# Kernel optimization log

Measured on AMD Instinct MI355X. Metric: run time of the kernel, lower is better.

Reference implementation:

```python
import jax, jax.numpy as jnp
import numpy as np

GAMMA = 0.99   # discount_factor
LAM = 0.95     # smoothing_factor

def setup_inputs() -> dict:
    key = jax.random.key(0)
    k1, k2, k3, k4 = jax.random.split(key, 4)
    B, T = 4096, 2048
    return {
        "rewards": jax.random.normal(k1, (B, T), dtype=jnp.float32),
        "values": jax.random.normal(k2, (B, T), dtype=jnp.float32),
        "next_value": jax.random.normal(k3, (B,), dtype=jnp.float32),
        "done_flags": jax.random.randint(k4, (B, T), 0, 2, dtype=jnp.int32),
    }

def reference(rewards, values, next_value, done_flags):
    d = done_flags.astype(rewards.dtype)
    # next_non_terminal[t] = 1 - done[t+1] for t < T-1, and 1 - done[T-1] at t = T-1
    nnt = 1.0 - jnp.concatenate([d[..., 1:], d[..., -1:]], axis=-1)
    # next value at step t: values[t+1] for t < T-1, bootstrap next_value at t = T-1
    nv = jnp.concatenate([values[..., 1:], next_value[..., None]], axis=-1)
    delta = rewards + GAMMA * nv * nnt - values  # [B, T]

    def step(gae, x):
        dl, nn = x
        gae = dl + GAMMA * LAM * nn * gae
        return gae, gae

    # scan backward over time (leading axis for lax.scan)
    deltaT = jnp.moveaxis(delta, -1, 0)  # [T, B]
    nntT = jnp.moveaxis(nnt, -1, 0)      # [T, B]
    init = jnp.zeros(rewards.shape[:-1], rewards.dtype)
    _, advT = jax.lax.scan(step, init, (deltaT, nntT), reverse=True)
    advantages = jnp.moveaxis(advT, 0, -1)  # [B, T]
    returns = advantages + values
    return advantages, returns
```

## Files before the change

### kernel.cpp

```cpp
#include <hip/hip_runtime.h>

#define GAMMA 0.99f
#define LAM   0.95f

typedef float v4f __attribute__((ext_vector_type(4)));
typedef int   v4i __attribute__((ext_vector_type(4)));

constexpr int CH   = 8;
constexpr int SEG  = 64 * CH;
constexpr int NSEG = 4;
constexpr int WPB  = 4;

struct Raw {
    v4f ra, rb, va, vb;
    v4i da, db;
};

__device__ __forceinline__ Raw load_seg(const float* __restrict__ r,
                                        const float* __restrict__ v,
                                        const int*   __restrict__ d,
                                        long base) {
    Raw x;
    x.ra = reinterpret_cast<const v4f*>(r + base)[0];
    x.rb = reinterpret_cast<const v4f*>(r + base)[1];
    x.va = reinterpret_cast<const v4f*>(v + base)[0];
    x.vb = reinterpret_cast<const v4f*>(v + base)[1];
    x.da = reinterpret_cast<const v4i*>(d + base)[0];
    x.db = reinterpret_cast<const v4i*>(d + base)[1];
    return x;
}

__device__ __forceinline__ void compute_seg(
    const Raw x, const int lane, const bool last_seg, const float nvrow,
    float& g, float& bv, int& bd,
    float* __restrict__ adv_out, float* __restrict__ ret_out, const long base)
{
    float r[CH] = {x.ra.x, x.ra.y, x.ra.z, x.ra.w, x.rb.x, x.rb.y, x.rb.z, x.rb.w};
    float v[CH] = {x.va.x, x.va.y, x.va.z, x.va.w, x.vb.x, x.vb.y, x.vb.z, x.vb.w};
    int   d[CH] = {x.da.x, x.da.y, x.da.z, x.da.w, x.db.x, x.db.y, x.db.z, x.db.w};

    int   dnext = __shfl_down(d[0], 1);
    float vnext = __shfl_down(v[0], 1);
    if (lane == 63) {
        dnext = last_seg ? d[CH - 1] : bd;
        vnext = last_seg ? nvrow     : bv;
    }
    const float bv_new = __shfl(v[0], 0);
    const int   bd_new = __shfl(d[0], 0);

    float delta[CH], c[CH];
#pragma unroll
    for (int j = 0; j < CH; ++j) {
        const int   dn  = (j < CH - 1) ? d[j + 1] : dnext;
        const float nv  = (j < CH - 1) ? v[j + 1] : vnext;
        const float nnt = dn ? 0.0f : 1.0f;
        delta[j] = r[j] + GAMMA * nv * nnt - v[j];
        c[j]     = dn ? 0.0f : (GAMMA * LAM);
    }

    float a = 0.0f, m = 1.0f;
#pragma unroll
    for (int j = CH - 1; j >= 0; --j) { a = delta[j] + c[j] * a; m = c[j] * m; }

    float sa = a, sm = m;
#pragma unroll
    for (int s = 1; s < 64; s <<= 1) {
        const float oa = __shfl_down(sa, s);
        const float om = __shfl_down(sm, s);
        if (lane + s < 64) { sa += sm * oa; sm *= om; }
    }
    float gin = __shfl_down(sa, 1);
    float em  = __shfl_down(sm, 1);
    if (lane == 63) { gin = 0.0f; em = 1.0f; }
    gin = gin + em * g;

    float adv[CH];
#pragma unroll
    for (int j = CH - 1; j >= 0; --j) { gin = delta[j] + c[j] * gin; adv[j] = gin; }

    v4f* a4 = reinterpret_cast<v4f*>(adv_out + base);
    v4f* t4 = reinterpret_cast<v4f*>(ret_out + base);
    v4f o0; o0.x = adv[0]; o0.y = adv[1]; o0.z = adv[2]; o0.w = adv[3];
    v4f o1; o1.x = adv[4]; o1.y = adv[5]; o1.z = adv[6]; o1.w = adv[7];
    v4f s0; s0.x = adv[0]+v[0]; s0.y = adv[1]+v[1]; s0.z = adv[2]+v[2]; s0.w = adv[3]+v[3];
    v4f s1; s1.x = adv[4]+v[4]; s1.y = adv[5]+v[5]; s1.z = adv[6]+v[6]; s1.w = adv[7]+v[7];
    a4[0] = o0; a4[1] = o1;
    t4[0] = s0; t4[1] = s1;

    g  = __shfl(gin, 0);
    bv = bv_new;
    bd = bd_new;
}

__global__ __launch_bounds__(256, 4) void gae_wave_seg_kernel(
    const float* __restrict__ rewards,
    const float* __restrict__ values,
    const float* __restrict__ next_value,
    const int*   __restrict__ done,
    float* __restrict__ adv_out,
    float* __restrict__ ret_out,
    int B, int T)
{
    const int tid  = threadIdx.x;
    const int lane = tid & 63;
    const int wave = tid >> 6;
    const int row  = blockIdx.x * WPB + wave;
    if (row >= B) return;

    const long rowbase = (long)row * T;
    const long laneoff = rowbase + lane * CH;

    Raw b3 = load_seg(rewards, values, done, laneoff + 3 * SEG);
    Raw b2 = load_seg(rewards, values, done, laneoff + 2 * SEG);
    const float nvrow = next_value[row];

    float g = 0.0f, bv = 0.0f;
    int   bd = 0;

    Raw b1 = load_seg(rewards, values, done, laneoff + 1 * SEG);
    compute_seg(b3, lane, true,  nvrow, g, bv, bd, adv_out, ret_out, laneoff + 3 * SEG);
    Raw b0 = load_seg(rewards, values, done, laneoff + 0 * SEG);
    compute_seg(b2, lane, false, nvrow, g, bv, bd, adv_out, ret_out, laneoff + 2 * SEG);
    compute_seg(b1, lane, false, nvrow, g, bv, bd, adv_out, ret_out, laneoff + 1 * SEG);
    compute_seg(b0, lane, false, nvrow, g, bv, bd, adv_out, ret_out, laneoff + 0 * SEG);
}

__global__ void gae_naive_kernel(
    const float* __restrict__ rewards,
    const float* __restrict__ values,
    const float* __restrict__ next_value,
    const int*   __restrict__ done,
    float* __restrict__ adv_out,
    float* __restrict__ ret_out,
    int B, int T)
{
    int row = blockIdx.x * blockDim.x + threadIdx.x;
    if (row >= B) return;
    long base = (long)row * T;
    float g = 0.0f;
    for (int t = T - 1; t >= 0; --t) {
        int dcol = (t + 1 < T) ? (t + 1) : (T - 1);
        float nnt = 1.0f - (float)done[base + dcol];
        float nv  = (t + 1 < T) ? values[base + t + 1] : next_value[row];
        float dl  = rewards[base + t] + GAMMA * nv * nnt - values[base + t];
        g = dl + (GAMMA * LAM) * nnt * g;
        adv_out[base + t] = g;
        ret_out[base + t] = g + values[base + t];
    }
}

extern "C" void kernel_launch(void* const* d_in, const int* in_sizes, int n_in,
                              void* d_out, int out_size, void* d_ws, size_t ws_size,
                              hipStream_t stream) {
    const float* rewards    = (const float*)d_in[0];
    const float* values     = (const float*)d_in[1];
    const float* next_value = (const float*)d_in[2];
    const int*   done       = (const int*)d_in[3];

    const int B = in_sizes[2];
    const int T = in_sizes[0] / B;

    float* adv = (float*)d_out;
    float* ret = adv + (long)B * T;

    if (T == NSEG * SEG) {
        const int grid = (B + WPB - 1) / WPB;
        gae_wave_seg_kernel<<<grid, 256, 0, stream>>>(
            rewards, values, next_value, done, adv, ret, B, T);
    } else {
        gae_naive_kernel<<<(B + 255) / 256, 256, 0, stream>>>(
            rewards, values, next_value, done, adv, ret, B, T);
    }
}
```

Before: 153.2 us.

## Process two rows per wavefront with interleaved segment scans for ILP

```diff
diff --git a/kernel.cpp b/kernel.cpp
--- a/kernel.cpp
+++ b/kernel.cpp
@@ -9,11 +9,17 @@
 constexpr int CH   = 8;
 constexpr int SEG  = 64 * CH;
 constexpr int NSEG = 4;
-constexpr int WPB  = 4;
+constexpr int RPW  = 2;
 
 struct Raw {
     v4f ra, rb, va, vb;
     v4i da, db;
+};
+
+struct RowState {
+    float g;
+    float bv;
+    int   bd;
 };
 
 __device__ __forceinline__ Raw load_seg(const float* __restrict__ r,
@@ -32,7 +38,7 @@
 
 __device__ __forceinline__ void compute_seg(
     const Raw x, const int lane, const bool last_seg, const float nvrow,
-    float& g, float& bv, int& bd,
+    RowState& st,
     float* __restrict__ adv_out, float* __restrict__ ret_out, const long base)
 {
     float r[CH] = {x.ra.x, x.ra.y, x.ra.z, x.ra.w, x.rb.x, x.rb.y, x.rb.z, x.rb.w};
@@ -42,8 +48,8 @@
     int   dnext = __shfl_down(d[0], 1);
     float vnext = __shfl_down(v[0], 1);
     if (lane == 63) {
-        dnext = last_seg ? d[CH - 1] : bd;
-        vnext = last_seg ? nvrow     : bv;
+        dnext = last_seg ? d[CH - 1] : st.bd;
+        vnext = last_seg ? nvrow     : st.bv;
     }
     const float bv_new = __shfl(v[0], 0);
     const int   bd_new = __shfl(d[0], 0);
@@ -72,7 +78,7 @@
     float gin = __shfl_down(sa, 1);
     float em  = __shfl_down(sm, 1);
     if (lane == 63) { gin = 0.0f; em = 1.0f; }
-    gin = gin + em * g;
+    gin = gin + em * st.g;
 
     float adv[CH];
 #pragma unroll
@@ -87,12 +93,12 @@
     a4[0] = o0; a4[1] = o1;
     t4[0] = s0; t4[1] = s1;
 
-    g  = __shfl(gin, 0);
-    bv = bv_new;
-    bd = bd_new;
+    st.g  = __shfl(gin, 0);
+    st.bv = bv_new;
+    st.bd = bd_new;
 }
 
-__global__ __launch_bounds__(256, 4) void gae_wave_seg_kernel(
+__global__ __launch_bounds__(256, 2) void gae_wave2_kernel(
     const float* __restrict__ rewards,
     const float* __restrict__ values,
     const float* __restrict__ next_value,
@@ -104,25 +110,39 @@
     const int tid  = threadIdx.x;
     const int lane = tid & 63;
     const int wave = tid >> 6;
-    const int row  = blockIdx.x * WPB + wave;
-    if (row >= B) return;
+    const int gw   = blockIdx.x * 4 + wave;
+    const int row0 = gw * RPW;
+    const int row1 = row0 + 1;
+    if (row0 >= B) return;
+    const bool has1 = (row1 < B);
 
-    const long rowbase = (long)row * T;
-    const long laneoff = rowbase + lane * CH;
+    const long off0 = (long)row0 * T + lane * CH;
+    const long off1 = (long)row1 * T + lane * CH;
 
-    Raw b3 = load_seg(rewards, values, done, laneoff + 3 * SEG);
-    Raw b2 = load_seg(rewards, values, done, laneoff + 2 * SEG);
-    const float nvrow = next_value[row];
+    Raw a3 = load_seg(rewards, values, done, off0 + 3 * SEG);
+    Raw b3 = has1 ? load_seg(rewards, values, done, off1 + 3 * SEG) : Raw{};
+    Raw a2 = load_seg(rewards, values, done, off0 + 2 * SEG);
+    Raw b2 = has1 ? load_seg(rewards, values, done, off1 + 2 * SEG) : Raw{};
+    const float nv0 = next_value[row0];
+    const float nv1 = has1 ? next_value[row1] : 0.0f;
 
-    float g = 0.0f, bv = 0.0f;
-    int   bd = 0;
+    RowState s0 = {0.0f, 0.0f, 0};
+    RowState s1 = {0.0f, 0.0f, 0};
 
-    Raw b1 = load_seg(rewards, values, done, laneoff + 1 * SEG);
-    compute_seg(b3, lane, true,  nvrow, g, bv, bd, adv_out, ret_out, laneoff + 3 * SEG);
-    Raw b0 = load_seg(rewards, values, done, laneoff + 0 * SEG);
-    compute_seg(b2, lane, false, nvrow, g, bv, bd, adv_out, ret_out, laneoff + 2 * SEG);
-    compute_seg(b1, lane, false, nvrow, g, bv, bd, adv_out, ret_out, laneoff + 1 * SEG);
-    compute_seg(b0, lane, false, nvrow, g, bv, bd, adv_out, ret_out, laneoff + 0 * SEG);
+    compute_seg(a3, lane, true, nv0, s0, adv_out, ret_out, off0 + 3 * SEG);
+    Raw a1 = load_seg(rewards, values, done, off0 + 1 * SEG);
+    if (has1) compute_seg(b3, lane, true, nv1, s1, adv_out, ret_out, off1 + 3 * SEG);
+    Raw b1 = has1 ? load_seg(rewards, values, done, off1 + 1 * SEG) : Raw{};
+
+    compute_seg(a2, lane, false, nv0, s0, adv_out, ret_out, off0 + 2 * SEG);
+    Raw a0 = load_seg(rewards, values, done, off0 + 0 * SEG);
+    if (has1) compute_seg(b2, lane, false, nv1, s1, adv_out, ret_out, off1 + 2 * SEG);
+    Raw b0 = has1 ? load_seg(rewards, values, done, off1 + 0 * SEG) : Raw{};
+
+    compute_seg(a1, lane, false, nv0, s0, adv_out, ret_out, off0 + 1 * SEG);
+    if (has1) compute_seg(b1, lane, false, nv1, s1, adv_out, ret_out, off1 + 1 * SEG);
+    compute_seg(a0, lane, false, nv0, s0, adv_out, ret_out, off0 + 0 * SEG);
+    if (has1) compute_seg(b0, lane, false, nv1, s1, adv_out, ret_out, off1 + 0 * SEG);
 }
 
 __global__ void gae_naive_kernel(
@@ -164,8 +184,9 @@
     float* ret = adv + (long)B * T;
 
     if (T == NSEG * SEG) {
-        const int grid = (B + WPB - 1) / WPB;
-        gae_wave_seg_kernel<<<grid, 256, 0, stream>>>(
+        const int nwaves = (B + RPW - 1) / RPW;
+        const int grid   = (nwaves + 3) / 4;
+        gae_wave2_kernel<<<grid, 256, 0, stream>>>(
             rewards, values, next_value, done, adv, ret, B, T);
     } else {
         gae_naive_kernel<<<(B + 255) / 256, 256, 0, stream>>>(
```

New measurement: 149.7 us. 1.02x faster.
